# Kernel optimization log

Measured on AMD Instinct MI355X. Metric: run time of the kernel, lower is better.

## Reference

```python
import jax, jax.numpy as jnp
import numpy as np

B, D, M = 512, 1024, 32768
K, MULTI_K, AUX_K = 32, 128, 64
DEAD_THRESH = 256
MATRYOSHKA_SIZES = [4096, 16384, 32768]


def setup_inputs() -> dict:
    key = jax.random.key(0)
    k0, k1, k2, k3, k4, k5 = jax.random.split(key, 6)
    return {
        "x": jax.random.normal(k0, (B, D), dtype=jnp.float32),
        "W_enc": jax.random.normal(k1, (M, D), dtype=jnp.float32) * 0.02,
        "W_dec": jax.random.normal(k2, (D, M), dtype=jnp.float32) * 0.02,
        "input_bias": jax.random.normal(k3, (D,), dtype=jnp.float32) * 0.01,
        "neuron_bias": jax.random.normal(k4, (M,), dtype=jnp.float32) * 0.01,
        "steps_since_activation": jax.random.randint(k5, (M,), 0, 512, dtype=jnp.int64),
    }


def reference(x, W_enc, W_dec, input_bias, neuron_bias, steps_since_activation):
    xc = x - input_bias                                   # [B, D]
    pre_act = xc @ W_enc.T + neuron_bias                  # [B, M]

    topk_values, topk_indices = jax.lax.top_k(pre_act, K)
    topk_values = jax.nn.relu(topk_values)
    multik_values, multik_indices = jax.lax.top_k(pre_act, MULTI_K)
    multik_values = jax.nn.relu(multik_values)

    rows = jnp.arange(pre_act.shape[0])[:, None]
    activations = jnp.zeros_like(pre_act).at[rows, topk_indices].set(topk_values)
    multik_activations = jnp.zeros_like(pre_act).at[rows, multik_indices].set(multik_values)

    reconstruction = activations @ W_dec.T + input_bias
    multik_reconstruction = multik_activations @ W_dec.T + input_bias

    # matryoshka partial reconstructions (all sizes except the last/full one)
    neuron_ids = jnp.arange(M)
    matryoshka_recons = []
    for m_i in MATRYOSHKA_SIZES[:-1]:
        partial_acts = activations * (neuron_ids < m_i).astype(activations.dtype)
        matryoshka_recons.append(partial_acts @ W_dec.T + input_bias)

    # aux-k over dead neurons (steps incremented by 1 before the mask in torch)
    dead_mask = ((steps_since_activation + 1) > DEAD_THRESH).astype(pre_act.dtype)
    aux_values, aux_indices = jax.lax.top_k(pre_act * dead_mask, AUX_K)
    aux_values = jax.nn.relu(aux_values)

    return (reconstruction, multik_reconstruction,
            matryoshka_recons[0], matryoshka_recons[1],
            topk_indices, topk_values, aux_indices, aux_values)
```

## Files before the change

kernel.cpp:

```cpp
#include <hip/hip_runtime.h>
#include <stdint.h>

#define B_ 512
#define D_ 1024
#define M_ 32768

typedef _Float16 half8 __attribute__((ext_vector_type(8)));
typedef _Float16 half4 __attribute__((ext_vector_type(4)));
typedef float f32x4 __attribute__((ext_vector_type(4)));

__device__ __forceinline__ unsigned f2k(float f) {
    unsigned b = __float_as_uint(f);
    return (b & 0x80000000u) ? ~b : (b | 0x80000000u);
}
__device__ __forceinline__ float k2f(unsigned k) {
    unsigned b = (k & 0x80000000u) ? (k & 0x7FFFFFFFu) : ~k;
    return __uint_as_float(b);
}
__device__ __forceinline__ unsigned long long d2k(double d) {
    unsigned long long b = (unsigned long long)__double_as_longlong(d);
    return (b & 0x8000000000000000ull) ? ~b : (b | 0x8000000000000000ull);
}

__device__ __forceinline__ void gld16(const void* g, void* l) {
    __builtin_amdgcn_global_load_lds(
        (__attribute__((address_space(1))) void*)(uintptr_t)g,
        (__attribute__((address_space(3))) void*)(unsigned)(uintptr_t)l,
        16, 0, 0);
}

__global__ __launch_bounds__(256) void split_x_k(
    const float* __restrict__ x, const float* __restrict__ ib,
    _Float16* __restrict__ xh)
{
    int i = blockIdx.x * 256 + threadIdx.x;
    float4 v = ((const float4*)x)[i];
    float4 bb = ((const float4*)ib)[i & 255];
    float a0 = (v.x - bb.x) * 2048.0f;
    float a1 = (v.y - bb.y) * 2048.0f;
    float a2 = (v.z - bb.z) * 2048.0f;
    float a3 = (v.w - bb.w) * 2048.0f;
    half4 hv = {(_Float16)a0, (_Float16)a1, (_Float16)a2, (_Float16)a3};
    ((half4*)xh)[i] = hv;
}

__global__ __launch_bounds__(256, 4) void enc_tr(
    const _Float16* __restrict__ xhf,
    const float* __restrict__ wenc, const float* __restrict__ nb,
    float* __restrict__ preact,
    const float* __restrict__ wdec, float* __restrict__ wdt)
{
    __shared__ alignas(16) _Float16 lA[2][128 * 32];
    __shared__ alignas(16) _Float16 lB[2][2][64 * 32];
    __shared__ float ttile[32][33];

    const int tid = threadIdx.x;
    const int chunk = blockIdx.x >> 8;
    const int sub = (chunk >> 1) * 256 + (blockIdx.x & 255);

    if (chunk & 1) {
        const int tx = tid & 31, ty = tid >> 5;
        for (int s = 0; s < 16; ++s) {
            int tix = sub * 16 + s;
            int x0 = (tix & 1023) * 32;
            int y0 = (tix >> 10) * 32;
#pragma unroll
            for (int j = 0; j < 32; j += 8)
                ttile[ty + j][tx] = wdec[(size_t)(y0 + ty + j) * M_ + x0 + tx];
            __syncthreads();
#pragma unroll
            for (int j = 0; j < 32; j += 8)
                wdt[(size_t)(x0 + ty + j) * D_ + y0 + tx] = ttile[tx][ty + j];
            __syncthreads();
        }
        return;
    }

    const int lane = tid & 63;
    const int wv = tid >> 6;
    const int wvr = wv >> 1;
    const int wvc = wv & 1;

    const int bid = sub;
    const int lb = bid >> 3;
    const int j0 = ((bid & 7) * 64 + (lb >> 2)) * 64;
    const int i0 = (lb & 3) * 128;

    const int ln15 = lane & 15;
    const int kq = (lane >> 4) * 8;

    f32x4 acc1[4][2], acc2[4][2];
#pragma unroll
    for (int r = 0; r < 4; ++r)
#pragma unroll
        for (int c = 0; c < 2; ++c) {
            acc1[r][c] = (f32x4){0.f, 0.f, 0.f, 0.f};
            acc2[r][c] = (f32x4){0.f, 0.f, 0.f, 0.f};
        }

    const int o0 = tid * 16;
    const int o1 = o0 + 4096;
    const int rA0 = o0 >> 6, rA1 = o1 >> 6;
    const int cA0s = (o0 & 63) ^ (((rA0 >> 1) & 3) << 4);
    const int cA1s = (o1 & 63) ^ (((rA1 >> 1) & 3) << 4);

    const int rW = tid >> 2;
    const int c8 = (tid & 3) * 8;
    const int c8s = c8 ^ (((rW >> 1) & 3) << 3);

    const int rowA = wvr * 64 + ln15;
    const int rowB = wvc * 32 + ln15;

#define STAGEA(k0, s)                                                                      \
    do {                                                                                   \
        gld16((const char*)(xhf + (size_t)(i0 + rA0) * 1024 + (k0)) + cA0s, (char*)lA[s] + o0); \
        gld16((const char*)(xhf + (size_t)(i0 + rA1) * 1024 + (k0)) + cA1s, (char*)lA[s] + o1); \
    } while (0)

#define LOADB(k0)                                                                          \
    do {                                                                                   \
        const float* wp = wenc + (size_t)(j0 + rW) * 1024 + (k0) + c8;                     \
        wv0 = *(const float4*)wp;                                                          \
        wv1 = *(const float4*)(wp + 4);                                                    \
    } while (0)

#define CVT1(idx, f)                                                                       \
    do { float a_ = (f) * 2048.0f; _Float16 h_ = (_Float16)a_;                             \
         bh[idx] = h_; br[idx] = (_Float16)((a_ - (float)h_) * 2048.0f); } while (0)

#define WRITEB(s)                                                                          \
    do {                                                                                   \
        half8 bh, br;                                                                      \
        CVT1(0, wv0.x); CVT1(1, wv0.y); CVT1(2, wv0.z); CVT1(3, wv0.w);                    \
        CVT1(4, wv1.x); CVT1(5, wv1.y); CVT1(6, wv1.z); CVT1(7, wv1.w);                    \
        *(half8*)&lB[s][0][rW * 32 + c8s] = bh;                                            \
        *(half8*)&lB[s][1][rW * 32 + c8s] = br;                                            \
    } while (0)

    float4 wv0, wv1;
    LOADB(0);
    asm volatile("s_waitcnt vmcnt(0)" ::: "memory");
    WRITEB(0);
    STAGEA(0, 0);
    LOADB(32);
    STAGEA(32, 1);
    asm volatile("s_waitcnt vmcnt(2)" ::: "memory");
    WRITEB(1);
    asm volatile("s_waitcnt lgkmcnt(0)" ::: "memory");
    __builtin_amdgcn_s_barrier();

    int cur = 0;
    for (int k0 = 0; k0 < 1024; k0 += 32) {
        if (k0 + 64 < 1024) LOADB(k0 + 64);

        half8 aH[4], bH[2], bR[2];
#pragma unroll
        for (int r = 0; r < 4; ++r) {
            const int ra = rowA + r * 16;
            const int ka = kq ^ (((ra >> 1) & 3) << 3);
            aH[r] = *(const half8*)&lA[cur][ra * 32 + ka];
        }
#pragma unroll
        for (int c = 0; c < 2; ++c) {
            const int rb = rowB + c * 16;
            const int kb = kq ^ (((rb >> 1) & 3) << 3);
            bH[c] = *(const half8*)&lB[cur][0][rb * 32 + kb];
            bR[c] = *(const half8*)&lB[cur][1][rb * 32 + kb];
        }
#pragma unroll
        for (int r = 0; r < 4; ++r)
#pragma unroll
            for (int c = 0; c < 2; ++c) {
                acc1[r][c] = __builtin_amdgcn_mfma_f32_16x16x32_f16(aH[r], bH[c], acc1[r][c], 0, 0, 0);
                acc2[r][c] = __builtin_amdgcn_mfma_f32_16x16x32_f16(aH[r], bR[c], acc2[r][c], 0, 0, 0);
            }

        if (k0 + 32 < 1024) {
            asm volatile("s_waitcnt lgkmcnt(0)" ::: "memory");
            __builtin_amdgcn_s_barrier();

            if (k0 + 64 < 1024) {
                STAGEA(k0 + 64, cur);
                asm volatile("s_waitcnt vmcnt(2)" ::: "memory");
                WRITEB(cur);
            } else {
                asm volatile("s_waitcnt vmcnt(0)" ::: "memory");
            }
            asm volatile("s_waitcnt lgkmcnt(0)" ::: "memory");
            __builtin_amdgcn_s_barrier();
        }
        cur ^= 1;
    }
#undef STAGEA
#undef LOADB
#undef CVT1
#undef WRITEB

    const float s1 = 0x1p-22f, s2 = 0x1p-33f;
#pragma unroll
    for (int c = 0; c < 2; ++c) {
        int n = j0 + wvc * 32 + c * 16 + ln15;
        float nbv = nb[n];
#pragma unroll
        for (int r = 0; r < 4; ++r) {
            int mb = i0 + wvr * 64 + r * 16 + (lane >> 4) * 4;
#pragma unroll
            for (int e = 0; e < 4; ++e)
                preact[(size_t)(mb + e) * M_ + n] = acc1[r][c][e] * s1 + acc2[r][c][e] * s2 + nbv;
        }
    }
}

__global__ __launch_bounds__(1024, 2) void selresdec(
    const float* __restrict__ preact, const int* __restrict__ steps,
    const float* __restrict__ x, const float* __restrict__ ib,
    const float* __restrict__ wenc, const float* __restrict__ nb,
    const float* __restrict__ wdt,
    float* __restrict__ out_tidx, float* __restrict__ out_tval,
    float* __restrict__ out_aidx, float* __restrict__ out_aval,
    float* __restrict__ o_recon, float* __restrict__ o_multik,
    float* __restrict__ o_mat0, float* __restrict__ o_mat1)
{
    __shared__ unsigned histU[4096];
    __shared__ unsigned histM[4096];
    __shared__ unsigned coarseU[256];
    __shared__ unsigned coarseM[256];
    __shared__ unsigned long long candU[512];
    __shared__ unsigned long long candM[512];
    __shared__ double xcs[1024];
    __shared__ double part[160][4];
    __shared__ unsigned long long kU[64];
    __shared__ unsigned long long kM[128];
    __shared__ float vU[64];
    __shared__ float vM[128];
    __shared__ int sidx[128];
    __shared__ float sval[128];
    __shared__ int auxm[96];
    __shared__ int ridx[32];
    __shared__ float rval[32];
    __shared__ unsigned cntU, cntM, thrU, thrM, cbU, cbM, cumU, cumM;

    const int t = threadIdx.x;
    const int b = blockIdx.x;
    const float* row = preact + (size_t)b * M_;

    for (int i = t; i < 4096; i += 1024) { histU[i] = 0; histM[i] = 0; }
    if (t < 512) { candU[t] = 0ULL; candM[t] = 0ULL; }
    if (t == 0) { cntU = 0; cntM = 0; }
    xcs[t] = (double)x[(size_t)b * 1024 + t] - (double)ib[t];
    if (t < 64)  { kU[t] = 0ULL; vU[t] = 0.f; }
    if (t < 128) { kM[t] = 0ULL; vM[t] = 0.f; }
    __syncthreads();

    unsigned deadmask = 0;
#pragma unroll
    for (int p = 0; p < 8; ++p) {
        int i = t + p * 1024;
        int4 sv = ((const int4*)steps)[i];
        unsigned mbits = 0;
        if (sv.x + 1 > 256) mbits |= 1u;
        if (sv.y + 1 > 256) mbits |= 2u;
        if (sv.z + 1 > 256) mbits |= 4u;
        if (sv.w + 1 > 256) mbits |= 8u;
        deadmask |= mbits << (p * 4);
    }

    float4 v[8];
#pragma unroll
    for (int p = 0; p < 8; ++p) {
        int i = t + p * 1024;
        v[p] = ((const float4*)row)[i];
        unsigned k0 = f2k(v[p].x) >> 20;
        unsigned k1 = f2k(v[p].y) >> 20;
        unsigned k2 = f2k(v[p].z) >> 20;
        unsigned k3 = f2k(v[p].w) >> 20;
        atomicAdd(&histU[k0], 1u);
        atomicAdd(&histU[k1], 1u);
        atomicAdd(&histU[k2], 1u);
        atomicAdd(&histU[k3], 1u);
        unsigned dm = deadmask >> (p * 4);
        if (dm & 1u) atomicAdd(&histM[k0], 1u);
        if (dm & 2u) atomicAdd(&histM[k1], 1u);
        if (dm & 4u) atomicAdd(&histM[k2], 1u);
        if (dm & 8u) atomicAdd(&histM[k3], 1u);
    }
    __syncthreads();

    if (t < 256) {
        unsigned s = 0;
#pragma unroll
        for (int j = 0; j < 16; ++j) s += histU[t * 16 + j];
        coarseU[t] = s;
    } else if (t < 512) {
        int c = t - 256;
        unsigned s = 0;
#pragma unroll
        for (int j = 0; j < 16; ++j) s += histM[c * 16 + j];
        coarseM[c] = s;
    }
    __syncthreads();

    for (int off = 1; off < 256; off <<= 1) {
        unsigned xv = 0;
        if (t < 256)      xv = coarseU[t] + (t + off < 256 ? coarseU[t + off] : 0u);
        else if (t < 512) { int c = t - 256; xv = coarseM[c] + (c + off < 256 ? coarseM[c + off] : 0u); }
        __syncthreads();
        if (t < 256)      coarseU[t] = xv;
        else if (t < 512) coarseM[t - 256] = xv;
        __syncthreads();
    }

    if (t < 256) {
        unsigned S = coarseU[t];
        unsigned Sn = (t < 255) ? coarseU[t + 1] : 0u;
        if (S >= 128u && (t == 255 || Sn < 128u)) { cbU = (unsigned)t; cumU = Sn; }
    } else if (t < 512) {
        int c = t - 256;
        unsigned S = coarseM[c];
        unsigned Sn = (c < 255) ? coarseM[c + 1] : 0u;
        if (S >= 64u && (c == 255 || Sn < 64u)) { cbM = (unsigned)c; cumM = Sn; }
        if (c == 0 && S < 64u) { cbM = 0u; cumM = Sn; }
    }
    __syncthreads();

    if (t == 0) {
        unsigned cum = cumU;
        int base = (int)cbU * 16, tb = base;
        for (int f = base + 15; f >= base; --f) {
            unsigned h = histU[f];
            if (cum + h >= 128u) { tb = f; break; }
            cum += h;
        }
        thrU = (unsigned)tb;
    }
    if (t == 64) {
        unsigned cum = cumM;
        int base = (int)cbM * 16, tb = base;
        for (int f = base + 15; f >= base; --f) {
            unsigned h = histM[f];
            if (cum + h >= 64u) { tb = f; break; }
            cum += h;
        }
        thrM = (unsigned)(tb > 0 ? tb - 1 : 0);
    }
    __syncthreads();

    const unsigned TU = thrU, TM = thrM;

#pragma unroll
    for (int p = 0; p < 8; ++p) {
        int i = t + p * 1024;
#pragma unroll
        for (int e = 0; e < 4; ++e) {
            float val = (e == 0) ? v[p].x : (e == 1) ? v[p].y : (e == 2) ? v[p].z : v[p].w;
            unsigned key = f2k(val);
            int m = i * 4 + e;
            if ((key >> 20) >= TU) {
                unsigned pz = atomicAdd(&cntU, 1u);
                if (pz < 512u) candU[pz] = ((unsigned long long)key << 32) | (unsigned)(~m);
            }
            if (((deadmask >> (p * 4 + e)) & 1u) && (key >> 20) >= TM) {
                unsigned pz = atomicAdd(&cntM, 1u);
                if (pz < 512u) candM[pz] = ((unsigned long long)key << 32) | (unsigned)(~m);
            }
        }
    }
    __syncthreads();

    {
        unsigned long long* arr = (t < 512) ? candU : candM;
        const unsigned i = (unsigned)t & 511u;
        for (unsigned kk = 2; kk <= 512; kk <<= 1) {
            for (unsigned j = kk >> 1; j > 0; j >>= 1) {
                unsigned ixj = i ^ j;
                if (ixj > i) {
                    bool desc = ((i & kk) == 0);
                    unsigned long long a = arr[i], c = arr[ixj];
                    if (desc ? (a < c) : (a > c)) { arr[i] = c; arr[ixj] = a; }
                }
                unsigned nj = (j > 1) ? (j >> 1) : ((kk << 1) <= 512u ? kk : 0u);
                if (j >= 64 || nj >= 64) __syncthreads();
                else asm volatile("s_waitcnt lgkmcnt(0)" ::: "memory");
            }
        }
    }
    __syncthreads();

    if (t < 128) {
        unsigned long long c = candU[t];
        unsigned m = ~(unsigned)c;
        float vv = k2f((unsigned)(c >> 32));
        sidx[t] = (int)m;
        sval[t] = vv > 0.f ? vv : 0.f;
    }
    if (t < 96) {
        unsigned long long c = candM[t];
        auxm[t] = c ? (int)(~(unsigned)c) : -1;
    }
    __syncthreads();

    if (t < 640) {
        const int ci = t >> 2, q = t & 3;
        int m = (ci < 64) ? sidx[ci] : auxm[ci - 64];
        if (m >= 0) {
            const float* w = wenc + (size_t)m * 1024 + q * 256;
            const double* xq = xcs + q * 256;
            double a0 = 0.0, a1 = 0.0, a2 = 0.0, a3 = 0.0;
            for (int d = 0; d < 256; d += 4) {
                float4 wv = *(const float4*)(w + d);
                a0 = fma((double)wv.x, xq[d + 0], a0);
                a1 = fma((double)wv.y, xq[d + 1], a1);
                a2 = fma((double)wv.z, xq[d + 2], a2);
                a3 = fma((double)wv.w, xq[d + 3], a3);
            }
            part[ci][q] = ((a0 + a1) + (a2 + a3));
        }
    }
    __syncthreads();

    if (t < 160) {
        int m = (t < 64) ? sidx[t] : auxm[t - 64];
        if (m >= 0) {
            double vd = ((part[t][0] + part[t][1]) + (part[t][2] + part[t][3])) + (double)nb[m];
            unsigned long long key = (d2k(vd) & 0xFFFFFFFFFFFF0000ull)
                                   | (unsigned long long)((~(unsigned)m) & 0xFFFFu);
            float vf = (float)vd;
            if (t < 64) { kU[t] = key; vU[t] = vf; }
            else        { kM[t - 64] = key; vM[t - 64] = vf; }
        }
    }
    __syncthreads();

    for (unsigned kk = 2; kk <= 128; kk <<= 1) {
        for (unsigned j = kk >> 1; j > 0; j >>= 1) {
            unsigned i = (unsigned)t, ixj = i ^ j;
            if (kk <= 64 && i < 64 && ixj > i) {
                bool desc = ((i & kk) == 0);
                unsigned long long a = kU[i], c = kU[ixj];
                if (desc ? (a < c) : (a > c)) {
                    kU[i] = c; kU[ixj] = a;
                    float fa = vU[i]; vU[i] = vU[ixj]; vU[ixj] = fa;
                }
            }
            if (i < 128 && ixj > i) {
                bool desc = ((i & kk) == 0);
                unsigned long long a = kM[i], c = kM[ixj];
                if (desc ? (a < c) : (a > c)) {
                    kM[i] = c; kM[ixj] = a;
                    float fa = vM[i]; vM[i] = vM[ixj]; vM[ixj] = fa;
                }
            }
            __syncthreads();
        }
    }

    if (t < 32) {
        unsigned mm = (~(unsigned)kU[t]) & 0xFFFFu;
        float vv = vU[t];
        float rv = vv > 0.f ? vv : 0.f;
        ridx[t] = (int)mm;
        rval[t] = rv;
        out_tidx[b * 32 + t] = (float)mm;
        out_tval[b * 32 + t] = rv;
    }
    if (t < 64) {
        unsigned mm = (~(unsigned)kM[t]) & 0xFFFFu;
        float vv = vM[t];
        out_aidx[b * 64 + t] = (float)mm;
        out_aval[b * 64 + t] = vv > 0.f ? vv : 0.f;
    }
    __syncthreads();

    {
        const int d = t;
        float bias = ib[d];
        float mul = bias, rec = bias, m0 = bias, m1 = bias;
        for (int k = 0; k < 128; ++k) {
            float vv = sval[k];
            float w = wdt[(size_t)sidx[k] * D_ + d];
            mul += vv * w;
        }
        for (int k = 0; k < 32; ++k) {
            int idx = ridx[k];
            float vv = rval[k];
            float w = wdt[(size_t)idx * D_ + d];
            rec += vv * w;
            if (idx < 16384) {
                m1 += vv * w;
                if (idx < 4096) m0 += vv * w;
            }
        }
        size_t o = (size_t)b * D_ + d;
        o_recon[o]  = rec;
        o_multik[o] = mul;
        o_mat0[o]   = m0;
        o_mat1[o]   = m1;
    }
}

extern "C" void kernel_launch(void* const* d_in, const int* in_sizes, int n_in,
                              void* d_out, int out_size, void* d_ws, size_t ws_size,
                              hipStream_t stream)
{
    const float* x     = (const float*)d_in[0];
    const float* wenc  = (const float*)d_in[1];
    const float* wdec  = (const float*)d_in[2];
    const float* ib    = (const float*)d_in[3];
    const float* nb    = (const float*)d_in[4];
    const int*   steps = (const int*)d_in[5];
    float* out = (float*)d_out;

    char* ws = (char*)d_ws;
    float*     preact  = (float*)ws;
    float*     wdt     = (float*)(ws + 67108864);
    _Float16*  xhf     = (_Float16*)(ws + 201326592);

    float* out_recon  = out;
    float* out_multik = out + 524288;
    float* out_mat0   = out + 1048576;
    float* out_mat1   = out + 1572864;
    float* out_tidx   = out + 2097152;
    float* out_tval   = out + 2097152 + 16384;
    float* out_aidx   = out + 2097152 + 32768;
    float* out_aval   = out + 2097152 + 32768 + 32768;

    split_x_k<<<dim3(512), dim3(256), 0, stream>>>(x, ib, xhf);
    enc_tr<<<dim3(4096), dim3(256), 0, stream>>>(xhf, wenc, nb, preact, wdec, wdt);
    selresdec<<<dim3(512), dim3(1024), 0, stream>>>(
        preact, steps, x, ib, wenc, nb, wdt,
        out_tidx, out_tval, out_aidx, out_aval,
        out_recon, out_multik, out_mat0, out_mat1);
}
```

Baseline: 541.2 us.

## Drop fp16 residual split in encoder and store pre-activations as fp16

The encoder GEMM no longer splits W_enc into a high and a residual fp16 part, so each tile issues one MFMA chain instead of two. The pre-activation matrix is now written and read as fp16, which halves its global-memory footprint. The selection kernel is adapted to load half8 vectors and build its histograms and candidates from them. Shared memory is folded into one buffer and the launch-bounds occupancy hint is raised from 4 to 6. The cost is lower encoder precision and coarser pre-activation values, which can change top-k ordering on near-ties unless the candidates are rescored exactly later.

```diff
diff --git a/kernel.cpp b/kernel.cpp
--- a/kernel.cpp
+++ b/kernel.cpp
@@ -44,21 +44,20 @@
     ((half4*)xh)[i] = hv;
 }
 
-__global__ __launch_bounds__(256, 4) void enc_tr(
+__global__ __launch_bounds__(256, 6) void enc_tr(
     const _Float16* __restrict__ xhf,
     const float* __restrict__ wenc, const float* __restrict__ nb,
-    float* __restrict__ preact,
+    _Float16* __restrict__ preact,
     const float* __restrict__ wdec, float* __restrict__ wdt)
 {
-    __shared__ alignas(16) _Float16 lA[2][128 * 32];
-    __shared__ alignas(16) _Float16 lB[2][2][64 * 32];
-    __shared__ float ttile[32][33];
+    __shared__ alignas(16) char smem[24576];
 
     const int tid = threadIdx.x;
     const int chunk = blockIdx.x >> 8;
     const int sub = (chunk >> 1) * 256 + (blockIdx.x & 255);
 
     if (chunk & 1) {
+        float (*ttile)[33] = (float(*)[33])smem;
         const int tx = tid & 31, ty = tid >> 5;
         for (int s = 0; s < 16; ++s) {
             int tix = sub * 16 + s;
@@ -76,6 +75,9 @@
         return;
     }
 
+    _Float16* lA0 = (_Float16*)smem;
+    _Float16* lB0 = (_Float16*)(smem + 16384);
+
     const int lane = tid & 63;
     const int wv = tid >> 6;
     const int wvr = wv >> 1;
@@ -89,14 +91,12 @@
     const int ln15 = lane & 15;
     const int kq = (lane >> 4) * 8;
 
-    f32x4 acc1[4][2], acc2[4][2];
+    f32x4 acc1[4][2];
 #pragma unroll
     for (int r = 0; r < 4; ++r)
 #pragma unroll
-        for (int c = 0; c < 2; ++c) {
+        for (int c = 0; c < 2; ++c)
             acc1[r][c] = (f32x4){0.f, 0.f, 0.f, 0.f};
-            acc2[r][c] = (f32x4){0.f, 0.f, 0.f, 0.f};
-        }
 
     const int o0 = tid * 16;
     const int o1 = o0 + 4096;
@@ -113,8 +113,8 @@
 
 #define STAGEA(k0, s)                                                                      \
     do {                                                                                   \
-        gld16((const char*)(xhf + (size_t)(i0 + rA0) * 1024 + (k0)) + cA0s, (char*)lA[s] + o0); \
-        gld16((const char*)(xhf + (size_t)(i0 + rA1) * 1024 + (k0)) + cA1s, (char*)lA[s] + o1); \
+        gld16((const char*)(xhf + (size_t)(i0 + rA0) * 1024 + (k0)) + cA0s, (char*)lA0 + (s) * 8192 + o0); \
+        gld16((const char*)(xhf + (size_t)(i0 + rA1) * 1024 + (k0)) + cA1s, (char*)lA0 + (s) * 8192 + o1); \
     } while (0)
 
 #define LOADB(k0)                                                                          \
@@ -124,17 +124,14 @@
         wv1 = *(const float4*)(wp + 4);                                                    \
     } while (0)
 
-#define CVT1(idx, f)                                                                       \
-    do { float a_ = (f) * 2048.0f; _Float16 h_ = (_Float16)a_;                             \
-         bh[idx] = h_; br[idx] = (_Float16)((a_ - (float)h_) * 2048.0f); } while (0)
+#define CVT1(idx, f) do { bh[idx] = (_Float16)((f) * 2048.0f); } while (0)
 
 #define WRITEB(s)                                                                          \
     do {                                                                                   \
-        half8 bh, br;                                                                      \
+        half8 bh;                                                                          \
         CVT1(0, wv0.x); CVT1(1, wv0.y); CVT1(2, wv0.z); CVT1(3, wv0.w);                    \
         CVT1(4, wv1.x); CVT1(5, wv1.y); CVT1(6, wv1.z); CVT1(7, wv1.w);                    \
-        *(half8*)&lB[s][0][rW * 32 + c8s] = bh;                                            \
-        *(half8*)&lB[s][1][rW * 32 + c8s] = br;                                            \
+        *(half8*)&lB0[(s) * 2048 + rW * 32 + c8s] = bh;                                    \
     } while (0)
 
     float4 wv0, wv1;
@@ -153,27 +150,24 @@
     for (int k0 = 0; k0 < 1024; k0 += 32) {
         if (k0 + 64 < 1024) LOADB(k0 + 64);
 
-        half8 aH[4], bH[2], bR[2];
+        half8 aH[4], bH[2];
 #pragma unroll
         for (int r = 0; r < 4; ++r) {
             const int ra = rowA + r * 16;
             const int ka = kq ^ (((ra >> 1) & 3) << 3);
-            aH[r] = *(const half8*)&lA[cur][ra * 32 + ka];
+            aH[r] = *(const half8*)&lA0[cur * 4096 + ra * 32 + ka];
         }
 #pragma unroll
         for (int c = 0; c < 2; ++c) {
             const int rb = rowB + c * 16;
             const int kb = kq ^ (((rb >> 1) & 3) << 3);
-            bH[c] = *(const half8*)&lB[cur][0][rb * 32 + kb];
-            bR[c] = *(const half8*)&lB[cur][1][rb * 32 + kb];
+            bH[c] = *(const half8*)&lB0[cur * 2048 + rb * 32 + kb];
         }
 #pragma unroll
         for (int r = 0; r < 4; ++r)
 #pragma unroll
-            for (int c = 0; c < 2; ++c) {
+            for (int c = 0; c < 2; ++c)
                 acc1[r][c] = __builtin_amdgcn_mfma_f32_16x16x32_f16(aH[r], bH[c], acc1[r][c], 0, 0, 0);
-                acc2[r][c] = __builtin_amdgcn_mfma_f32_16x16x32_f16(aH[r], bR[c], acc2[r][c], 0, 0, 0);
-            }
 
         if (k0 + 32 < 1024) {
             asm volatile("s_waitcnt lgkmcnt(0)" ::: "memory");
@@ -196,7 +190,7 @@
 #undef CVT1
 #undef WRITEB
 
-    const float s1 = 0x1p-22f, s2 = 0x1p-33f;
+    const float s1 = 0x1p-22f;
 #pragma unroll
     for (int c = 0; c < 2; ++c) {
         int n = j0 + wvc * 32 + c * 16 + ln15;
@@ -206,13 +200,13 @@
             int mb = i0 + wvr * 64 + r * 16 + (lane >> 4) * 4;
 #pragma unroll
             for (int e = 0; e < 4; ++e)
-                preact[(size_t)(mb + e) * M_ + n] = acc1[r][c][e] * s1 + acc2[r][c][e] * s2 + nbv;
+                preact[(size_t)(mb + e) * M_ + n] = (_Float16)(acc1[r][c][e] * s1 + nbv);
         }
     }
 }
 
 __global__ __launch_bounds__(1024, 2) void selresdec(
-    const float* __restrict__ preact, const int* __restrict__ steps,
+    const _Float16* __restrict__ preact, const int* __restrict__ steps,
     const float* __restrict__ x, const float* __restrict__ ib,
     const float* __restrict__ wenc, const float* __restrict__ nb,
     const float* __restrict__ wdt,
@@ -242,7 +236,7 @@
 
     const int t = threadIdx.x;
     const int b = blockIdx.x;
-    const float* row = preact + (size_t)b * M_;
+    const half8* rowh = (const half8*)(preact + (size_t)b * M_);
 
     for (int i = t; i < 4096; i += 1024) { histU[i] = 0; histM[i] = 0; }
     if (t < 512) { candU[t] = 0ULL; candM[t] = 0ULL; }
@@ -254,35 +248,32 @@
 
     unsigned deadmask = 0;
 #pragma unroll
-    for (int p = 0; p < 8; ++p) {
-        int i = t + p * 1024;
-        int4 sv = ((const int4*)steps)[i];
-        unsigned mbits = 0;
-        if (sv.x + 1 > 256) mbits |= 1u;
-        if (sv.y + 1 > 256) mbits |= 2u;
-        if (sv.z + 1 > 256) mbits |= 4u;
-        if (sv.w + 1 > 256) mbits |= 8u;
-        deadmask |= mbits << (p * 4);
-    }
-
-    float4 v[8];
-#pragma unroll
-    for (int p = 0; p < 8; ++p) {
-        int i = t + p * 1024;
-        v[p] = ((const float4*)row)[i];
-        unsigned k0 = f2k(v[p].x) >> 20;
-        unsigned k1 = f2k(v[p].y) >> 20;
-        unsigned k2 = f2k(v[p].z) >> 20;
-        unsigned k3 = f2k(v[p].w) >> 20;
-        atomicAdd(&histU[k0], 1u);
-        atomicAdd(&histU[k1], 1u);
-        atomicAdd(&histU[k2], 1u);
-        atomicAdd(&histU[k3], 1u);
-        unsigned dm = deadmask >> (p * 4);
-        if (dm & 1u) atomicAdd(&histM[k0], 1u);
-        if (dm & 2u) atomicAdd(&histM[k1], 1u);
-        if (dm & 4u) atomicAdd(&histM[k2], 1u);
-        if (dm & 8u) atomicAdd(&histM[k3], 1u);
+    for (int p = 0; p < 4; ++p) {
+        int base = 2 * t + 2048 * p;
+        int4 s0 = ((const int4*)steps)[base];
+        int4 s1 = ((const int4*)steps)[base + 1];
+        unsigned mb = 0;
+        if (s0.x + 1 > 256) mb |= 1u;
+        if (s0.y + 1 > 256) mb |= 2u;
+        if (s0.z + 1 > 256) mb |= 4u;
+        if (s0.w + 1 > 256) mb |= 8u;
+        if (s1.x + 1 > 256) mb |= 16u;
+        if (s1.y + 1 > 256) mb |= 32u;
+        if (s1.z + 1 > 256) mb |= 64u;
+        if (s1.w + 1 > 256) mb |= 128u;
+        deadmask |= mb << (p * 8);
+    }
+
+    half8 v[4];
+#pragma unroll
+    for (int p = 0; p < 4; ++p) {
+        v[p] = rowh[t + p * 1024];
+#pragma unroll
+        for (int e = 0; e < 8; ++e) {
+            unsigned key = f2k((float)v[p][e]) >> 20;
+            atomicAdd(&histU[key], 1u);
+            if ((deadmask >> (p * 8 + e)) & 1u) atomicAdd(&histM[key], 1u);
+        }
     }
     __syncthreads();
 
@@ -348,18 +339,17 @@
     const unsigned TU = thrU, TM = thrM;
 
 #pragma unroll
-    for (int p = 0; p < 8; ++p) {
-        int i = t + p * 1024;
-#pragma unroll
-        for (int e = 0; e < 4; ++e) {
-            float val = (e == 0) ? v[p].x : (e == 1) ? v[p].y : (e == 2) ? v[p].z : v[p].w;
+    for (int p = 0; p < 4; ++p) {
+#pragma unroll
+        for (int e = 0; e < 8; ++e) {
+            float val = (float)v[p][e];
             unsigned key = f2k(val);
-            int m = i * 4 + e;
+            int m = (t + p * 1024) * 8 + e;
             if ((key >> 20) >= TU) {
                 unsigned pz = atomicAdd(&cntU, 1u);
                 if (pz < 512u) candU[pz] = ((unsigned long long)key << 32) | (unsigned)(~m);
             }
-            if (((deadmask >> (p * 4 + e)) & 1u) && (key >> 20) >= TM) {
+            if (((deadmask >> (p * 8 + e)) & 1u) && (key >> 20) >= TM) {
                 unsigned pz = atomicAdd(&cntM, 1u);
                 if (pz < 512u) candM[pz] = ((unsigned long long)key << 32) | (unsigned)(~m);
             }
@@ -511,7 +501,7 @@
     float* out = (float*)d_out;
 
     char* ws = (char*)d_ws;
-    float*     preact  = (float*)ws;
+    _Float16*  preact  = (_Float16*)ws;
     float*     wdt     = (float*)(ws + 67108864);
     _Float16*  xhf     = (_Float16*)(ws + 201326592);
 
```

Result: no change. 533.6 us (-1.4%).
